# Optimization experiments

Hardware: AMD Instinct MI355X
Metric: run time of the kernel (lower is better)

The kernel has to match this reference:

```python
import jax, jax.numpy as jnp
import numpy as np

N, E, G = 100000, 3200000, 5000
EPS = 1e-5
HEADS, HC = 8, 16


def setup_inputs() -> dict:
    key = jax.random.key(0)
    k = jax.random.split(key, 12)

    def lin(kk, fi, fo):
        return (jax.random.normal(kk, (fi, fo), jnp.float32) / np.sqrt(fi)).astype(jnp.float32)

    return {
        "x": jax.random.normal(k[0], (N, 20), jnp.float32),
        "edge_index": jax.random.randint(k[1], (2, E), 0, N, dtype=jnp.int32),
        "batch": jnp.sort(jax.random.randint(k[2], (N,), 0, G, dtype=jnp.int32)),
        "W1": lin(k[3], 20, 64), "b1": jnp.zeros((64,), jnp.float32),
        "g1": jnp.ones((64,), jnp.float32), "be1": jnp.zeros((64,), jnp.float32),
        "W2": lin(k[4], 64, 32), "b2": jnp.zeros((32,), jnp.float32),
        "g2": jnp.ones((32,), jnp.float32), "be2": jnp.zeros((32,), jnp.float32),
        "W3": lin(k[5], 32, 16), "b3": jnp.zeros((16,), jnp.float32),
        "g3": jnp.ones((16,), jnp.float32), "be3": jnp.zeros((16,), jnp.float32),
        "Wg": lin(k[6], 16, HEADS * HC),
        "att_src": jax.random.normal(k[7], (HEADS, HC), jnp.float32) * 0.1,
        "att_dst": jax.random.normal(k[8], (HEADS, HC), jnp.float32) * 0.1,
        "bg": jnp.zeros((HC,), jnp.float32),
        "Wf": lin(k[9], 16, 3), "bf": jnp.zeros((3,), jnp.float32),
    }


def reference(x, edge_index, batch,
              W1, b1, g1, be1, W2, b2, g2, be2, W3, b3, g3, be3,
              Wg, att_src, att_dst, bg, Wf, bf):
    src, dst = edge_index[0], edge_index[1]
    loop = jnp.arange(N, dtype=src.dtype)
    src_sl = jnp.concatenate([src, loop])  # self-loops (GCN + GAT add_self_loops)
    dst_sl = jnp.concatenate([dst, loop])

    # GCN symmetric normalization D^-1/2 (A+I) D^-1/2
    deg = jax.ops.segment_sum(jnp.ones_like(src_sl, dtype=jnp.float32), dst_sl, N)
    dinv = jnp.where(deg > 0, 1.0 / jnp.sqrt(deg), 0.0)
    norm = (dinv[src_sl] * dinv[dst_sl])[:, None]  # [E+N, 1]

    def gcn(h, W, b):
        h = h @ W
        return jax.ops.segment_sum(h[src_sl] * norm, dst_sl, N) + b

    def bn_relu(h, g, b):  # BatchNorm1d (train-mode batch stats) + ReLU
        mu = h.mean(0)
        var = ((h - mu) ** 2).mean(0)
        return jax.nn.relu(g * (h - mu) * jax.lax.rsqrt(var + EPS) + b)

    h = bn_relu(gcn(x, W1, b1), g1, be1)   # dropout = identity (eval)
    h = bn_relu(gcn(h, W2, b2), g2, be2)
    h = bn_relu(gcn(h, W3, b3), g3, be3)

    # GATConv: heads=8, concat=False (mean over heads), eval -> no dropout
    xg = (h @ Wg).reshape(N, HEADS, HC)
    a_src = (xg * att_src).sum(-1)  # [N, H]
    a_dst = (xg * att_dst).sum(-1)
    logit = jax.nn.leaky_relu(a_src[src_sl] + a_dst[dst_sl], 0.2)  # [E+N, H]
    m = jax.ops.segment_max(logit, dst_sl, N)          # segment softmax over dst
    e = jnp.exp(logit - m[dst_sl])
    s = jax.ops.segment_sum(e, dst_sl, N)
    alpha = e / s[dst_sl]
    agg = jax.ops.segment_sum(xg[src_sl] * alpha[:, :, None], dst_sl, N)  # [N,H,C]
    hg = agg.mean(1) + bg  # [N, 16]

    pooled = jax.ops.segment_sum(hg, batch, G)  # global_add_pool -> [G, 16]
    return pooled @ Wf + bf  # [G, 3]
```

## Files before the change

kernel.cpp:

```cpp
#include <hip/hip_runtime.h>
#include <hip/hip_fp16.h>

constexpr int NN = 100000;
constexpr int EE = 3200000;
constexpr int GG = 5000;
constexpr float BNEPS = 1e-5f;

constexpr int BINS = 128;
constexpr int NPB = (NN + BINS - 1) / BINS;
constexpr int BCHUNK = 8192;
constexpr int NBCH = (EE + BCHUNK - 1) / BCHUNK;
constexpr int BINCAP2 = 96;
constexpr int BINREG = 27648;
constexpr int LCAP = 26624;
constexpr int CTR_STRIDE = 32;

typedef int int4v __attribute__((ext_vector_type(4)));


__global__ __launch_bounds__(1024) void bin_edges(const int* __restrict__ ei,
                                                  uint2* __restrict__ pairs,
                                                  int* __restrict__ binCur) {
    __shared__ int bcnt[BINS];
    __shared__ int bbase[BINS];
    __shared__ uint2 buf[BINS][BINCAP2];
    const int t = threadIdx.x;
    const int lane = t & 63, wv = t >> 6;
    for (int ch = blockIdx.x; ch < NBCH; ch += gridDim.x) {
        for (int k = t; k < BINS; k += 1024) bcnt[k] = 0;
        __syncthreads();
        const int qbase = ch * (BCHUNK / 4);
#pragma unroll
        for (int rep = 0; rep < 2; ++rep) {
            const int q = qbase + rep * 1024 + t;
            if (q < EE / 4) {
                int4v d = __builtin_nontemporal_load((const int4v*)(ei + EE) + q);
                int4v s = __builtin_nontemporal_load((const int4v*)ei + q);
                int dd[4] = {d.x, d.y, d.z, d.w};
                int ss[4] = {s.x, s.y, s.z, s.w};
#pragma unroll
                for (int k = 0; k < 4; ++k) {
                    int o = dd[k] / NPB;
                    int p = atomicAdd(&bcnt[o], 1);
                    if (p < BINCAP2) {
                        buf[o][p] = make_uint2((unsigned)dd[k], (unsigned)ss[k]);
                    } else {
                        int gp = atomicAdd(&binCur[o * CTR_STRIDE], 1);
                        pairs[(size_t)o * BINREG + gp] =
                            make_uint2((unsigned)dd[k], (unsigned)ss[k]);
                    }
                }
            }
        }
        __syncthreads();
        if (t < BINS) {
            int c = bcnt[t] < BINCAP2 ? bcnt[t] : BINCAP2;
            bbase[t] = atomicAdd(&binCur[t * CTR_STRIDE], c);
            bcnt[t] = c;
        }
        __syncthreads();
        for (int o = wv; o < BINS; o += 16) {
            const int c = bcnt[o];
            const size_t base = (size_t)o * BINREG + bbase[o];
            for (int k = lane; k < c; k += 64) pairs[base + k] = buf[o][k];
        }
        __syncthreads();
    }
}


__global__ void bin_base(const int* __restrict__ binCur, int* __restrict__ binBase) {
    __shared__ int s[BINS];
    const int t = threadIdx.x;
    const int v = binCur[t * CTR_STRIDE];
    s[t] = v;
    __syncthreads();
    for (int off = 1; off < BINS; off <<= 1) {
        int add = (t >= off) ? s[t - off] : 0;
        __syncthreads();
        s[t] += add;
        __syncthreads();
    }
    binBase[t] = s[t] - v;
}


__global__ __launch_bounds__(1024) void scatter_lds(const uint2* __restrict__ pairs,
                                                    const int* __restrict__ binCur,
                                                    const int* __restrict__ binBase,
                                                    int* __restrict__ rowptr,
                                                    float* __restrict__ dinv,
                                                    int* __restrict__ colA) {
    __shared__ int scnt[NPB];
    __shared__ int sscan[1024];
    __shared__ int lbuf[LCAP];
    const int b = blockIdx.x;
    const int t = threadIdx.x;
    const int lo = b * NPB;
    const int hi = (lo + NPB < NN) ? lo + NPB : NN;
    const int nb = hi - lo;
    const int tot = binCur[b * CTR_STRIDE];
    const int base = binBase[b];
    const uint2* p = pairs + (size_t)b * BINREG;
    for (int k = t; k < nb; k += 1024) scnt[k] = 0;
    __syncthreads();
    for (int q = t; q < tot; q += 1024) atomicAdd(&scnt[p[q].x - lo], 1);
    __syncthreads();
    const int myc = (t < nb) ? scnt[t] : 0;
    sscan[t] = myc;
    __syncthreads();
    for (int off = 1; off < 1024; off <<= 1) {
        int add = (t >= off) ? sscan[t - off] : 0;
        __syncthreads();
        sscan[t] += add;
        __syncthreads();
    }
    const int excl = sscan[t] - myc;
    if (t < nb) {
        rowptr[lo + t] = base + excl;
        dinv[lo + t] = rsqrtf((float)(myc + 1));
        scnt[t] = excl;
    }
    if (b == BINS - 1 && t == 0) rowptr[NN] = base + tot;
    __syncthreads();
    for (int q = t; q < tot; q += 1024) {
        uint2 e = p[q];
        int pos = atomicAdd(&scnt[e.x - lo], 1);
        if (pos < LCAP) lbuf[pos] = (int)e.y;
        else colA[base + pos] = (int)e.y;
    }
    __syncthreads();
    const int m = tot < LCAP ? tot : LCAP;
    for (int k = t; k < m; k += 1024) colA[base + k] = lbuf[k];
}


__global__ void scale_x(const float* __restrict__ x, const float* __restrict__ dinv,
                        __half* __restrict__ xsc) {
    int idx = blockIdx.x * blockDim.x + threadIdx.x;
    if (idx < NN * 20) {
        int n = idx / 20;
        xsc[idx] = __float2half(x[idx] * dinv[n]);
    }
}


template <int FIN, int FOUT, bool AFFINE, bool SCALED, bool STATS>
__global__ void gemm_k(const float* __restrict__ hin,
                       const float* __restrict__ sumsIn, const float* __restrict__ ssqIn,
                       const float* __restrict__ g, const float* __restrict__ be,
                       const float* __restrict__ W, const float* __restrict__ dinv,
                       const float* __restrict__ bias,
                       float* __restrict__ outF, __half* __restrict__ outH,
                       float* __restrict__ sumsOut, float* __restrict__ ssqOut) {
    constexpr int NB = 256 / FOUT;
    __shared__ float Wl[FIN * FOUT];
    __shared__ float rows[NB][FIN];
    __shared__ float aa[AFFINE ? FIN : 1], bb[AFFINE ? FIN : 1];
    const int t = threadIdx.x;
    if constexpr (AFFINE) {
        if (t < FIN) {
            float mu = sumsIn[t] / (float)NN;
            float var = ssqIn[t] / (float)NN - mu * mu;
            float a = g[t] * rsqrtf(var + BNEPS);
            aa[t] = a;
            bb[t] = be[t] - mu * a;
        }
    }
    for (int i = t; i < FIN * FOUT; i += 256) Wl[i] = W[i];
    const int c = t % FOUT, s = t / FOUT;
    const int ngrp = (NN + NB - 1) / NB;
    float sAcc = 0.f, qAcc = 0.f;
    for (int grp = blockIdx.x; grp < ngrp; grp += gridDim.x) {
        __syncthreads();
        for (int i = t; i < NB * FIN; i += 256) {
            int sn = i / FIN, k = i % FIN;
            int n2 = grp * NB + sn;
            float v = 0.f;
            if (n2 < NN) {
                v = hin[(size_t)n2 * FIN + k];
                if constexpr (AFFINE) {
                    v = aa[k] * v + bb[k];
                    v = v > 0.f ? v : 0.f;
                }
            }
            rows[sn][k] = v;
        }
        __syncthreads();
        int node = grp * NB + s;
        if (node < NN) {
            float acc = 0.f;
#pragma unroll
            for (int k = 0; k < FIN; ++k) acc += rows[s][k] * Wl[k * FOUT + c];
            if constexpr (SCALED) {
                outH[(size_t)node * FOUT + c] = __float2half(acc * dinv[node]);
            } else {
                float val = acc + bias[c];
                outF[(size_t)node * FOUT + c] = val;
                if constexpr (STATS) { sAcc += val; qAcc += val * val; }
            }
        }
    }
    if constexpr (STATS) {
        __shared__ float ls[FOUT], lq[FOUT];
        __syncthreads();
        if (t < FOUT) { ls[t] = 0.f; lq[t] = 0.f; }
        __syncthreads();
        atomicAdd(&ls[c], sAcc);
        atomicAdd(&lq[c], qAcc);
        __syncthreads();
        if (t < FOUT) { atomicAdd(&sumsOut[t], ls[t]); atomicAdd(&ssqOut[t], lq[t]); }
    }
}


template <int H2, int OUTF, bool STATS>
__global__ void agg_half(const __half2* __restrict__ src, const int* __restrict__ rowptr,
                         const int* __restrict__ colA, const float* __restrict__ dinv,
                         const float* __restrict__ bias, float* __restrict__ out,
                         float* __restrict__ sumsOut, float* __restrict__ ssqOut) {
    constexpr int SUB = 64 / H2;
    const int lane = threadIdx.x & 63;
    const int wid = (blockIdx.x * blockDim.x + threadIdx.x) >> 6;
    const int totalWaves = (gridDim.x * blockDim.x) >> 6;
    const int f = lane % H2;
    const int sub = lane / H2;
    const int stride = totalWaves * SUB;
    float bx = 0.f, by = 0.f;
    if (bias != nullptr) {
        bx = bias[2 * f];
        by = (2 * f + 1 < OUTF) ? bias[2 * f + 1] : 0.f;
    }
    const int i0 = (sub < SUB) ? wid * SUB + sub : NN;
    float sx = 0.f, qx = 0.f, sy = 0.f, qy = 0.f;
    for (int i = i0; i < NN; i += stride) {
        const int r0 = rowptr[i], r1 = rowptr[i + 1];
        float2 acc = __half22float2(src[(size_t)i * H2 + f]);
        float2 acc2 = {0.f, 0.f};
        int e = r0;
        for (; e + 3 < r1; e += 4) {
            int j0 = colA[e], j1 = colA[e + 1], j2 = colA[e + 2], j3 = colA[e + 3];
            float2 v0 = __half22float2(src[(size_t)j0 * H2 + f]);
            float2 v1 = __half22float2(src[(size_t)j1 * H2 + f]);
            float2 v2 = __half22float2(src[(size_t)j2 * H2 + f]);
            float2 v3 = __half22float2(src[(size_t)j3 * H2 + f]);
            acc.x += v0.x + v1.x;
            acc.y += v0.y + v1.y;
            acc2.x += v2.x + v3.x;
            acc2.y += v2.y + v3.y;
        }
        for (; e < r1; ++e) {
            float2 v = __half22float2(src[(size_t)colA[e] * H2 + f]);
            acc.x += v.x; acc.y += v.y;
        }
        acc.x += acc2.x; acc.y += acc2.y;
        const float d = dinv[i];
        float vx = d * acc.x + bx;
        out[(size_t)i * OUTF + 2 * f] = vx;
        if constexpr (STATS) { sx += vx; qx += vx * vx; }
        if (2 * f + 1 < OUTF) {
            float vy = d * acc.y + by;
            out[(size_t)i * OUTF + 2 * f + 1] = vy;
            if constexpr (STATS) { sy += vy; qy += vy * vy; }
        }
    }
    if constexpr (STATS) {
        __shared__ float ls[OUTF], lq[OUTF];
        const int t = threadIdx.x;
        if (t < OUTF) { ls[t] = 0.f; lq[t] = 0.f; }
        __syncthreads();
        atomicAdd(&ls[2 * f], sx);
        atomicAdd(&lq[2 * f], qx);
        if (2 * f + 1 < OUTF) {
            atomicAdd(&ls[2 * f + 1], sy);
            atomicAdd(&lq[2 * f + 1], qy);
        }
        __syncthreads();
        if (t < OUTF) { atomicAdd(&sumsOut[t], ls[t]); atomicAdd(&ssqOut[t], lq[t]); }
    }
}


__global__ void gat_mats(const float* __restrict__ Wg, const float* __restrict__ att_src,
                         const float* __restrict__ att_dst, const float* __restrict__ Wf,
                         const float* __restrict__ bg, float* __restrict__ Psrc,
                         float* __restrict__ Pdst, float* __restrict__ M,
                         float* __restrict__ bgW) {
    int t = threadIdx.x;
    if (t < 128) {
        int k = t >> 3, h = t & 7;
        float s = 0.f, d = 0.f;
        for (int c = 0; c < 16; ++c) {
            float wv = Wg[k * 128 + h * 16 + c];
            s += wv * att_src[h * 16 + c];
            d += wv * att_dst[h * 16 + c];
        }
        Psrc[k * 8 + h] = s;
        Pdst[k * 8 + h] = d;
    } else if (t < 512) {
        int m = t - 128;
        if (m < 384) {
            int hk = m / 3, j = m - hk * 3;
            int H = hk >> 4, k = hk & 15;
            float s = 0.f;
            for (int c = 0; c < 16; ++c) s += Wg[k * 128 + H * 16 + c] * Wf[c * 3 + j];
            M[hk * 3 + j] = 0.125f * s;
        }
    } else if (t < 515) {
        int j = t - 512;
        float s = 0.f;
        for (int c = 0; c < 16; ++c) s += bg[c] * Wf[c * 3 + j];
        bgW[j] = s;
    }
}


__global__ void gat_pre3(const float* __restrict__ h3,
                         const float* __restrict__ sums3, const float* __restrict__ ssq3,
                         const float* __restrict__ g3, const float* __restrict__ be3,
                         const float* __restrict__ Psrc, const float* __restrict__ Pdst,
                         __half* __restrict__ zc, float* __restrict__ adst) {
    __shared__ float Ps[128], Pd[128], aa[16], bb[16];
    int t = threadIdx.x;
    if (t < 128) { Ps[t] = Psrc[t]; Pd[t] = Pdst[t]; }
    if (t < 16) {
        float mu = sums3[t] / (float)NN;
        float var = ssq3[t] / (float)NN - mu * mu;
        float a = g3[t] * rsqrtf(var + BNEPS);
        aa[t] = a;
        bb[t] = be3[t] - mu * a;
    }
    __syncthreads();
    int n = blockIdx.x * blockDim.x + t;
    if (n >= NN) return;
    float zv[16];
#pragma unroll
    for (int k = 0; k < 16; ++k) {
        float v = h3[(size_t)n * 16 + k];
        v = aa[k] * v + bb[k];
        zv[k] = v > 0.f ? v : 0.f;
    }
    float as[8], ad[8];
#pragma unroll
    for (int h = 0; h < 8; ++h) { as[h] = 0.f; ad[h] = 0.f; }
#pragma unroll
    for (int k = 0; k < 16; ++k) {
        float zk = zv[k];
#pragma unroll
        for (int h = 0; h < 8; ++h) {
            as[h] += zk * Ps[k * 8 + h];
            ad[h] += zk * Pd[k * 8 + h];
        }
    }
    __half2 ah[4];
#pragma unroll
    for (int k = 0; k < 4; ++k) ah[k] = __floats2half2_rn(as[2 * k], as[2 * k + 1]);
    __half2 zh[8];
#pragma unroll
    for (int k = 0; k < 8; ++k) zh[k] = __floats2half2_rn(zv[2 * k], zv[2 * k + 1]);
    __half* row = zc + (size_t)n * 32;
    *(float4*)(row) = *(float4*)ah;
    *(float4*)(row + 8) = ((float4*)zh)[0];
    *(float4*)(row + 16) = ((float4*)zh)[1];
    float4* d4 = (float4*)(adst + (size_t)n * 8);
    d4[0] = make_float4(ad[0], ad[1], ad[2], ad[3]);
    d4[1] = make_float4(ad[4], ad[5], ad[6], ad[7]);
}


__device__ __forceinline__ float leaky02(float x) { return x > 0.f ? x : 0.2f * x; }

__global__ void gat_agg7(const __half* __restrict__ zc, const float* __restrict__ adst,
                         const int* __restrict__ rowptr, const int* __restrict__ colA,
                         __half* __restrict__ Sn) {
    const int lane = threadIdx.x & 63;
    const int q = lane & 3;
    const int hh = (lane >> 2) & 1;
    const int sub = lane >> 3;
    const int head = lane & 7;
    const int wid = (blockIdx.x * blockDim.x + threadIdx.x) >> 6;
    const int totalWaves = (gridDim.x * blockDim.x) >> 6;
    const int zoff = 8 + q * 4;
    for (int i = wid; i < NN; i += totalWaves) {
        const int r0 = rowptr[i], r1 = rowptr[i + 1];
        const float adh = adst[(size_t)i * 8 + head];
        float acc[4][4];
        float wsum[4];
        {
            const __half* row = zc + (size_t)i * 32;
            float aval = __half2float(row[head]);
            float wo = (sub == 0) ? __expf(leaky02(aval + adh)) : 0.f;
            float w1 = __shfl_xor(wo, 1);
            float w2 = __shfl_xor(wo, 2);
            float w3 = __shfl_xor(w1, 2);
            float w[4] = {wo, w1, w2, w3};
            float2 zraw = *(const float2*)(row + zoff);
            const __half2* zp = (const __half2*)&zraw;
            float2 f0 = __half22float2(zp[0]), f1 = __half22float2(zp[1]);
            float zf[4] = {f0.x, f0.y, f1.x, f1.y};
#pragma unroll
            for (int j = 0; j < 4; ++j) {
                wsum[j] = w[j];
#pragma unroll
                for (int k = 0; k < 4; ++k) acc[j][k] = w[j] * zf[k];
            }
        }
        for (int e = r0; e < r1; e += 16) {
            const int ee0 = e + sub, ee1 = e + 8 + sub;
            const bool v0 = ee0 < r1, v1 = ee1 < r1;
            const int j0 = v0 ? colA[ee0] : i;
            const int j1 = v1 ? colA[ee1] : i;
            const __half* row0 = zc + (size_t)j0 * 32;
            const __half* row1 = zc + (size_t)j1 * 32;
            float a0 = __half2float(row0[head]);
            float2 zraw0 = *(const float2*)(row0 + zoff);
            float a1 = __half2float(row1[head]);
            float2 zraw1 = *(const float2*)(row1 + zoff);
            {
                float wo = v0 ? __expf(leaky02(a0 + adh)) : 0.f;
                float w1 = __shfl_xor(wo, 1);
                float w2 = __shfl_xor(wo, 2);
                float w3 = __shfl_xor(w1, 2);
                float w[4] = {wo, w1, w2, w3};
                const __half2* zp = (const __half2*)&zraw0;
                float2 f0 = __half22float2(zp[0]), f1 = __half22float2(zp[1]);
                float zf[4] = {f0.x, f0.y, f1.x, f1.y};
#pragma unroll
                for (int j = 0; j < 4; ++j) {
                    wsum[j] += w[j];
#pragma unroll
                    for (int k = 0; k < 4; ++k) acc[j][k] += w[j] * zf[k];
                }
            }
            {
                float wo = v1 ? __expf(leaky02(a1 + adh)) : 0.f;
                float w1 = __shfl_xor(wo, 1);
                float w2 = __shfl_xor(wo, 2);
                float w3 = __shfl_xor(w1, 2);
                float w[4] = {wo, w1, w2, w3};
                const __half2* zp = (const __half2*)&zraw1;
                float2 f0 = __half22float2(zp[0]), f1 = __half22float2(zp[1]);
                float zf[4] = {f0.x, f0.y, f1.x, f1.y};
#pragma unroll
                for (int j = 0; j < 4; ++j) {
                    wsum[j] += w[j];
#pragma unroll
                    for (int k = 0; k < 4; ++k) acc[j][k] += w[j] * zf[k];
                }
            }
        }
#pragma unroll
        for (int off = 8; off < 64; off <<= 1) {
#pragma unroll
            for (int j = 0; j < 4; ++j) {
                wsum[j] += __shfl_xor(wsum[j], off);
#pragma unroll
                for (int k = 0; k < 4; ++k) acc[j][k] += __shfl_xor(acc[j][k], off);
            }
        }
        if (lane < 8) {
#pragma unroll
            for (int j = 0; j < 4; ++j) {
                const int hd = hh * 4 + (q ^ j);
                const float inv = 1.f / wsum[j];
                __half2 o[2];
                o[0] = __floats2half2_rn(acc[j][0] * inv, acc[j][1] * inv);
                o[1] = __floats2half2_rn(acc[j][2] * inv, acc[j][3] * inv);
                *(float2*)(Sn + (size_t)i * 128 + hd * 16 + q * 4) = *(float2*)o;
            }
        }
    }
}


__global__ void graph_bounds(const int* __restrict__ batch, int* __restrict__ gstart) {
    int n = blockIdx.x * blockDim.x + threadIdx.x;
    if (n < NN) {
        int bn = batch[n];
        int bp = (n == 0) ? -1 : batch[n - 1];
        for (int g = bp + 1; g <= bn; ++g) gstart[g] = n;
        if (n == NN - 1)
            for (int g = bn + 1; g <= GG; ++g) gstart[g] = NN;
    }
}


__global__ void pool_final(const __half2* __restrict__ Sn2, const int* __restrict__ gstart,
                           const float* __restrict__ M, const float* __restrict__ bgW,
                           const float* __restrict__ bf, float* __restrict__ out) {
    const int lane = threadIdx.x & 63;
    const int g = (blockIdx.x * blockDim.x + threadIdx.x) >> 6;
    if (g >= GG) return;
    const int n0 = gstart[g], n1 = gstart[g + 1];
    float2 s = {0.f, 0.f};
    for (int n = n0; n < n1; ++n) {
        float2 v = __half22float2(Sn2[(size_t)n * 64 + lane]);
        s.x += v.x;
        s.y += v.y;
    }
    float o[3];
#pragma unroll
    for (int j = 0; j < 3; ++j)
        o[j] = s.x * M[(2 * lane) * 3 + j] + s.y * M[(2 * lane + 1) * 3 + j];
#pragma unroll
    for (int off = 1; off < 64; off <<= 1) {
#pragma unroll
        for (int j = 0; j < 3; ++j) o[j] += __shfl_xor(o[j], off);
    }
    if (lane == 0) {
        float cnt = (float)(n1 - n0);
#pragma unroll
        for (int j = 0; j < 3; ++j) out[g * 3 + j] = o[j] + cnt * bgW[j] + bf[j];
    }
}


extern "C" void kernel_launch(void* const* d_in, const int* in_sizes, int n_in,
                              void* d_out, int out_size, void* d_ws, size_t ws_size,
                              hipStream_t stream) {
    const float* x = (const float*)d_in[0];
    const int* ei = (const int*)d_in[1];
    const int* batch = (const int*)d_in[2];
    const float* W1 = (const float*)d_in[3];  const float* b1 = (const float*)d_in[4];
    const float* g1 = (const float*)d_in[5];  const float* be1 = (const float*)d_in[6];
    const float* W2 = (const float*)d_in[7];  const float* b2 = (const float*)d_in[8];
    const float* g2 = (const float*)d_in[9];  const float* be2 = (const float*)d_in[10];
    const float* W3 = (const float*)d_in[11]; const float* b3 = (const float*)d_in[12];
    const float* g3 = (const float*)d_in[13]; const float* be3 = (const float*)d_in[14];
    const float* Wg = (const float*)d_in[15];
    const float* att_src = (const float*)d_in[16];
    const float* att_dst = (const float*)d_in[17];
    const float* bg = (const float*)d_in[18];
    const float* Wf = (const float*)d_in[19];
    const float* bf = (const float*)d_in[20];
    float* out = (float*)d_out;

    char* w = (char*)d_ws;
    auto alloc = [&](size_t bytes) -> char* {
        char* p = w;
        w += (bytes + 255) & ~(size_t)255;
        return p;
    };
    int* binCur = (int*)alloc((size_t)BINS * CTR_STRIDE * 4);
    float* sums1 = (float*)alloc(64 * 4); float* ssq1 = (float*)alloc(64 * 4);
    float* sums2 = (float*)alloc(32 * 4); float* ssq2 = (float*)alloc(32 * 4);
    float* sums3 = (float*)alloc(16 * 4); float* ssq3 = (float*)alloc(16 * 4);
    size_t zeroBytes = (size_t)(w - (char*)d_ws);
    int* binBase = (int*)alloc((size_t)BINS * 4);
    float* Psrc = (float*)alloc(128 * 4);
    float* Pdst = (float*)alloc(128 * 4);
    float* Mm = (float*)alloc(384 * 4);
    float* bgW = (float*)alloc(3 * 4);
    int* gstart = (int*)alloc((size_t)(GG + 1) * 4);
    int* rowptr = (int*)alloc((size_t)(NN + 1) * 4);
    int* colA = (int*)alloc((size_t)EE * 4);
    float* dinv = (float*)alloc((size_t)NN * 4);
    char* A = alloc((size_t)NN * 64 * 4);
    char* B = alloc((size_t)NN * 64 * 4);

    uint2*  pairs = (uint2*)A;
    __half* xsc  = (__half*)B;
    float*  aggx = (float*)(B + (size_t)NN * 32 * 2);
    float*  h1   = (float*)A;
    __half* hs2  = (__half*)B;
    float*  h2   = (float*)(B + (size_t)NN * 32 * 2);
    __half* hs3  = (__half*)A;
    float*  h3   = (float*)(A + (size_t)NN * 16 * 2);
    __half* zc   = (__half*)(A + (size_t)NN * 24 * 4);
    float*  adst = (float*)(A + (size_t)NN * 40 * 4);
    __half* Sn   = (__half*)B;

    hipMemsetAsync(d_ws, 0, zeroBytes, stream);

    bin_edges<<<256, 1024, 0, stream>>>(ei, pairs, binCur);
    bin_base<<<1, BINS, 0, stream>>>(binCur, binBase);
    scatter_lds<<<BINS, 1024, 0, stream>>>(pairs, binCur, binBase, rowptr, dinv, colA);
    gat_mats<<<1, 1024, 0, stream>>>(Wg, att_src, att_dst, Wf, bg, Psrc, Pdst, Mm, bgW);
    graph_bounds<<<(NN + 255) / 256, 256, 0, stream>>>(batch, gstart);

    scale_x<<<(NN * 20 + 255) / 256, 256, 0, stream>>>(x, dinv, xsc);
    agg_half<10, 20, false><<<2048, 256, 0, stream>>>((const __half2*)xsc, rowptr, colA, dinv,
                                                      nullptr, aggx, nullptr, nullptr);
    gemm_k<20, 64, false, false, true><<<2048, 256, 0, stream>>>(
        aggx, nullptr, nullptr, nullptr, nullptr, W1, dinv, b1, h1, nullptr, sums1, ssq1);

    gemm_k<64, 32, true, true, false><<<2048, 256, 0, stream>>>(
        h1, sums1, ssq1, g1, be1, W2, dinv, nullptr, nullptr, hs2, nullptr, nullptr);
    agg_half<16, 32, true><<<2048, 256, 0, stream>>>((const __half2*)hs2, rowptr, colA, dinv,
                                                     b2, h2, sums2, ssq2);

    gemm_k<32, 16, true, true, false><<<2048, 256, 0, stream>>>(
        h2, sums2, ssq2, g2, be2, W3, dinv, nullptr, nullptr, hs3, nullptr, nullptr);
    agg_half<8, 16, true><<<2048, 256, 0, stream>>>((const __half2*)hs3, rowptr, colA, dinv,
                                                    b3, h3, sums3, ssq3);

    gat_pre3<<<(NN + 255) / 256, 256, 0, stream>>>(h3, sums3, ssq3, g3, be3, Psrc, Pdst,
                                                   zc, adst);
    gat_agg7<<<2048, 256, 0, stream>>>(zc, adst, rowptr, colA, Sn);
    pool_final<<<(GG * 64 + 255) / 256, 256, 0, stream>>>((const __half2*)Sn, gstart, Mm, bgW,
                                                          bf, out);
}
```

Baseline: 525.1 us.

## Split neighbor aggregations into two source-half passes for cache locality

Each dst row's column list is now partitioned during CSR construction into sources below and above the node midpoint, with a new mid pointer array. Every GCN aggregation and the GAT aggregation run as two passes, one per source half, so each pass's random gathers touch only half of the feature table and can stay resident in L2. The second pass reads back the partial sums (and the GAT softmax weight partials) before normalizing. Outputs are now written with nontemporal stores. In exchange there are extra kernel launches, an extra read-modify-write of the outputs, and a second walk over row bounds.

```diff
diff --git a/kernel.cpp b/kernel.cpp
--- a/kernel.cpp
+++ b/kernel.cpp
@@ -4,6 +4,7 @@
 constexpr int NN = 100000;
 constexpr int EE = 3200000;
 constexpr int GG = 5000;
+constexpr int HALF = 50000;
 constexpr float BNEPS = 1e-5f;
 
 constexpr int BINS = 128;
@@ -16,6 +17,7 @@
 constexpr int CTR_STRIDE = 32;
 
 typedef int int4v __attribute__((ext_vector_type(4)));
+typedef float f2v __attribute__((ext_vector_type(2)));
 
 
 __global__ __launch_bounds__(1024) void bin_edges(const int* __restrict__ ei,
@@ -89,9 +91,11 @@
                                                     const int* __restrict__ binCur,
                                                     const int* __restrict__ binBase,
                                                     int* __restrict__ rowptr,
+                                                    int* __restrict__ mid,
                                                     float* __restrict__ dinv,
                                                     int* __restrict__ colA) {
     __shared__ int scnt[NPB];
+    __shared__ int scntA[NPB];
     __shared__ int sscan[1024];
     __shared__ int lbuf[LCAP];
     const int b = blockIdx.x;
@@ -102,9 +106,14 @@
     const int tot = binCur[b * CTR_STRIDE];
     const int base = binBase[b];
     const uint2* p = pairs + (size_t)b * BINREG;
-    for (int k = t; k < nb; k += 1024) scnt[k] = 0;
+    for (int k = t; k < nb; k += 1024) { scnt[k] = 0; scntA[k] = 0; }
     __syncthreads();
-    for (int q = t; q < tot; q += 1024) atomicAdd(&scnt[p[q].x - lo], 1);
+    for (int q = t; q < tot; q += 1024) {
+        uint2 e = p[q];
+        int d = (int)e.x - lo;
+        atomicAdd(&scnt[d], 1);
+        if ((int)e.y < HALF) atomicAdd(&scntA[d], 1);
+    }
     __syncthreads();
     const int myc = (t < nb) ? scnt[t] : 0;
     sscan[t] = myc;
@@ -117,15 +126,19 @@
     }
     const int excl = sscan[t] - myc;
     if (t < nb) {
+        int cA = scntA[t];
         rowptr[lo + t] = base + excl;
+        mid[lo + t] = base + excl + cA;
         dinv[lo + t] = rsqrtf((float)(myc + 1));
         scnt[t] = excl;
+        scntA[t] = excl + cA;
     }
     if (b == BINS - 1 && t == 0) rowptr[NN] = base + tot;
     __syncthreads();
     for (int q = t; q < tot; q += 1024) {
         uint2 e = p[q];
-        int pos = atomicAdd(&scnt[e.x - lo], 1);
+        int d = (int)e.x - lo;
+        int pos = ((int)e.y < HALF) ? atomicAdd(&scnt[d], 1) : atomicAdd(&scntA[d], 1);
         if (pos < LCAP) lbuf[pos] = (int)e.y;
         else colA[base + pos] = (int)e.y;
     }
@@ -214,11 +227,12 @@
 }
 
 
-template <int H2, int OUTF, bool STATS>
-__global__ void agg_half(const __half2* __restrict__ src, const int* __restrict__ rowptr,
-                         const int* __restrict__ colA, const float* __restrict__ dinv,
-                         const float* __restrict__ bias, float* __restrict__ out,
-                         float* __restrict__ sumsOut, float* __restrict__ ssqOut) {
+template <int H2, int OUTF, bool STATS, bool ACCUM>
+__global__ void agg_half(const __half2* __restrict__ src, const int* __restrict__ loArr,
+                         const int* __restrict__ hiArr, const int* __restrict__ colA,
+                         const float* __restrict__ dinv, const float* __restrict__ bias,
+                         float* __restrict__ out, float* __restrict__ sumsOut,
+                         float* __restrict__ ssqOut, int passIdx) {
     constexpr int SUB = 64 / H2;
     const int lane = threadIdx.x & 63;
     const int wid = (blockIdx.x * blockDim.x + threadIdx.x) >> 6;
@@ -234,8 +248,10 @@
     const int i0 = (sub < SUB) ? wid * SUB + sub : NN;
     float sx = 0.f, qx = 0.f, sy = 0.f, qy = 0.f;
     for (int i = i0; i < NN; i += stride) {
-        const int r0 = rowptr[i], r1 = rowptr[i + 1];
-        float2 acc = __half22float2(src[(size_t)i * H2 + f]);
+        const int r0 = loArr[i], r1 = hiArr[i];
+        float2 acc = {0.f, 0.f};
+        if ((i < HALF) == (passIdx == 0))
+            acc = __half22float2(src[(size_t)i * H2 + f]);
         float2 acc2 = {0.f, 0.f};
         int e = r0;
         for (; e + 3 < r1; e += 4) {
@@ -254,14 +270,20 @@
             acc.x += v.x; acc.y += v.y;
         }
         acc.x += acc2.x; acc.y += acc2.y;
-        const float d = dinv[i];
-        float vx = d * acc.x + bx;
-        out[(size_t)i * OUTF + 2 * f] = vx;
-        if constexpr (STATS) { sx += vx; qx += vx * vx; }
-        if (2 * f + 1 < OUTF) {
-            float vy = d * acc.y + by;
-            out[(size_t)i * OUTF + 2 * f + 1] = vy;
-            if constexpr (STATS) { sy += vy; qy += vy * vy; }
+        if constexpr (!ACCUM) {
+            __builtin_nontemporal_store(acc.x, &out[(size_t)i * OUTF + 2 * f]);
+            if (2 * f + 1 < OUTF)
+                __builtin_nontemporal_store(acc.y, &out[(size_t)i * OUTF + 2 * f + 1]);
+        } else {
+            const float d = dinv[i];
+            float vx = d * (acc.x + out[(size_t)i * OUTF + 2 * f]) + bx;
+            __builtin_nontemporal_store(vx, &out[(size_t)i * OUTF + 2 * f]);
+            if constexpr (STATS) { sx += vx; qx += vx * vx; }
+            if (2 * f + 1 < OUTF) {
+                float vy = d * (acc.y + out[(size_t)i * OUTF + 2 * f + 1]) + by;
+                __builtin_nontemporal_store(vy, &out[(size_t)i * OUTF + 2 * f + 1]);
+                if constexpr (STATS) { sy += vy; qy += vy * vy; }
+            }
         }
     }
     if constexpr (STATS) {
@@ -370,9 +392,11 @@
 
 __device__ __forceinline__ float leaky02(float x) { return x > 0.f ? x : 0.2f * x; }
 
-__global__ void gat_agg7(const __half* __restrict__ zc, const float* __restrict__ adst,
-                         const int* __restrict__ rowptr, const int* __restrict__ colA,
-                         __half* __restrict__ Sn) {
+template <bool ACCUM>
+__global__ void gat_agg8(const __half* __restrict__ zc, const float* __restrict__ adst,
+                         const int* __restrict__ loArr, const int* __restrict__ hiArr,
+                         const int* __restrict__ colA, __half* __restrict__ Sn,
+                         float* __restrict__ wsumP, int passIdx) {
     const int lane = threadIdx.x & 63;
     const int q = lane & 3;
     const int hh = (lane >> 2) & 1;
@@ -382,14 +406,15 @@
     const int totalWaves = (gridDim.x * blockDim.x) >> 6;
     const int zoff = 8 + q * 4;
     for (int i = wid; i < NN; i += totalWaves) {
-        const int r0 = rowptr[i], r1 = rowptr[i + 1];
+        const int r0 = loArr[i], r1 = hiArr[i];
         const float adh = adst[(size_t)i * 8 + head];
         float acc[4][4];
         float wsum[4];
         {
+            const bool selfHere = ((i < HALF) == (passIdx == 0)) && (sub == 0);
             const __half* row = zc + (size_t)i * 32;
             float aval = __half2float(row[head]);
-            float wo = (sub == 0) ? __expf(leaky02(aval + adh)) : 0.f;
+            float wo = selfHere ? __expf(leaky02(aval + adh)) : 0.f;
             float w1 = __shfl_xor(wo, 1);
             float w2 = __shfl_xor(wo, 2);
             float w3 = __shfl_xor(w1, 2);
@@ -459,14 +484,40 @@
             }
         }
         if (lane < 8) {
-#pragma unroll
-            for (int j = 0; j < 4; ++j) {
-                const int hd = hh * 4 + (q ^ j);
-                const float inv = 1.f / wsum[j];
-                __half2 o[2];
-                o[0] = __floats2half2_rn(acc[j][0] * inv, acc[j][1] * inv);
-                o[1] = __floats2half2_rn(acc[j][2] * inv, acc[j][3] * inv);
-                *(float2*)(Sn + (size_t)i * 128 + hd * 16 + q * 4) = *(float2*)o;
+            if constexpr (!ACCUM) {
+#pragma unroll
+                for (int j = 0; j < 4; ++j) {
+                    const int hd = hh * 4 + (q ^ j);
+                    __half2 o[2];
+                    o[0] = __floats2half2_rn(acc[j][0], acc[j][1]);
+                    o[1] = __floats2half2_rn(acc[j][2], acc[j][3]);
+                    f2v tv; tv.x = ((float*)o)[0]; tv.y = ((float*)o)[1];
+                    __builtin_nontemporal_store(tv,
+                        (f2v*)(Sn + (size_t)i * 128 + hd * 16 + q * 4));
+                }
+                if (q == 0) {
+#pragma unroll
+                    for (int j = 0; j < 4; ++j)
+                        __builtin_nontemporal_store(wsum[j],
+                                                    &wsumP[(size_t)i * 8 + hh * 4 + j]);
+                }
+            } else {
+#pragma unroll
+                for (int j = 0; j < 4; ++j) {
+                    const int hd = hh * 4 + (q ^ j);
+                    float2 praw = *(const float2*)(Sn + (size_t)i * 128 + hd * 16 + q * 4);
+                    const __half2* pp = (const __half2*)&praw;
+                    float2 p0 = __half22float2(pp[0]), p1 = __half22float2(pp[1]);
+                    const float inv = 1.f / (wsum[j] + wsumP[(size_t)i * 8 + hd]);
+                    __half2 o[2];
+                    o[0] = __floats2half2_rn((acc[j][0] + p0.x) * inv,
+                                             (acc[j][1] + p0.y) * inv);
+                    o[1] = __floats2half2_rn((acc[j][2] + p1.x) * inv,
+                                             (acc[j][3] + p1.y) * inv);
+                    f2v tv; tv.x = ((float*)o)[0]; tv.y = ((float*)o)[1];
+                    __builtin_nontemporal_store(tv,
+                        (f2v*)(Sn + (size_t)i * 128 + hd * 16 + q * 4));
+                }
             }
         }
     }
@@ -553,6 +604,7 @@
     float* bgW = (float*)alloc(3 * 4);
     int* gstart = (int*)alloc((size_t)(GG + 1) * 4);
     int* rowptr = (int*)alloc((size_t)(NN + 1) * 4);
+    int* midp = (int*)alloc((size_t)NN * 4);
     int* colA = (int*)alloc((size_t)EE * 4);
     float* dinv = (float*)alloc((size_t)NN * 4);
     char* A = alloc((size_t)NN * 64 * 4);
@@ -568,35 +620,43 @@
     float*  h3   = (float*)(A + (size_t)NN * 16 * 2);
     __half* zc   = (__half*)(A + (size_t)NN * 24 * 4);
     float*  adst = (float*)(A + (size_t)NN * 40 * 4);
+    float*  wsumP = (float*)(A + (size_t)NN * 48 * 4);
     __half* Sn   = (__half*)B;
 
     hipMemsetAsync(d_ws, 0, zeroBytes, stream);
 
     bin_edges<<<256, 1024, 0, stream>>>(ei, pairs, binCur);
     bin_base<<<1, BINS, 0, stream>>>(binCur, binBase);
-    scatter_lds<<<BINS, 1024, 0, stream>>>(pairs, binCur, binBase, rowptr, dinv, colA);
+    scatter_lds<<<BINS, 1024, 0, stream>>>(pairs, binCur, binBase, rowptr, midp, dinv, colA);
     gat_mats<<<1, 1024, 0, stream>>>(Wg, att_src, att_dst, Wf, bg, Psrc, Pdst, Mm, bgW);
     graph_bounds<<<(NN + 255) / 256, 256, 0, stream>>>(batch, gstart);
 
     scale_x<<<(NN * 20 + 255) / 256, 256, 0, stream>>>(x, dinv, xsc);
-    agg_half<10, 20, false><<<2048, 256, 0, stream>>>((const __half2*)xsc, rowptr, colA, dinv,
-                                                      nullptr, aggx, nullptr, nullptr);
+    agg_half<10, 20, false, false><<<2048, 256, 0, stream>>>(
+        (const __half2*)xsc, rowptr, midp, colA, dinv, nullptr, aggx, nullptr, nullptr, 0);
+    agg_half<10, 20, false, true><<<2048, 256, 0, stream>>>(
+        (const __half2*)xsc, midp, rowptr + 1, colA, dinv, nullptr, aggx, nullptr, nullptr, 1);
     gemm_k<20, 64, false, false, true><<<2048, 256, 0, stream>>>(
         aggx, nullptr, nullptr, nullptr, nullptr, W1, dinv, b1, h1, nullptr, sums1, ssq1);
 
     gemm_k<64, 32, true, true, false><<<2048, 256, 0, stream>>>(
         h1, sums1, ssq1, g1, be1, W2, dinv, nullptr, nullptr, hs2, nullptr, nullptr);
-    agg_half<16, 32, true><<<2048, 256, 0, stream>>>((const __half2*)hs2, rowptr, colA, dinv,
-                                                     b2, h2, sums2, ssq2);
+    agg_half<16, 32, false, false><<<2048, 256, 0, stream>>>(
+        (const __half2*)hs2, rowptr, midp, colA, dinv, nullptr, h2, nullptr, nullptr, 0);
+    agg_half<16, 32, true, true><<<2048, 256, 0, stream>>>(
+        (const __half2*)hs2, midp, rowptr + 1, colA, dinv, b2, h2, sums2, ssq2, 1);
 
     gemm_k<32, 16, true, true, false><<<2048, 256, 0, stream>>>(
         h2, sums2, ssq2, g2, be2, W3, dinv, nullptr, nullptr, hs3, nullptr, nullptr);
-    agg_half<8, 16, true><<<2048, 256, 0, stream>>>((const __half2*)hs3, rowptr, colA, dinv,
-                                                    b3, h3, sums3, ssq3);
+    agg_half<8, 16, false, false><<<2048, 256, 0, stream>>>(
+        (const __half2*)hs3, rowptr, midp, colA, dinv, nullptr, h3, nullptr, nullptr, 0);
+    agg_half<8, 16, true, true><<<2048, 256, 0, stream>>>(
+        (const __half2*)hs3, midp, rowptr + 1, colA, dinv, b3, h3, sums3, ssq3, 1);
 
     gat_pre3<<<(NN + 255) / 256, 256, 0, stream>>>(h3, sums3, ssq3, g3, be3, Psrc, Pdst,
                                                    zc, adst);
-    gat_agg7<<<2048, 256, 0, stream>>>(zc, adst, rowptr, colA, Sn);
+    gat_agg8<false><<<2048, 256, 0, stream>>>(zc, adst, rowptr, midp, colA, Sn, wsumP, 0);
+    gat_agg8<true><<<2048, 256, 0, stream>>>(zc, adst, midp, rowptr + 1, colA, Sn, wsumP, 1);
     pool_final<<<(GG * 64 + 255) / 256, 256, 0, stream>>>((const __half2*)Sn, gstart, Mm, bgW,
                                                           bf, out);
 }
```

Measured after the change: 642.4 us. 22.3% more time.
